# Kernel tuning notes

Hardware: AMD Instinct MI355X
Metric: run time of the kernel (lower is better)

Reference implementation:

```python
import jax, jax.numpy as jnp
import numpy as np
import math

N_QUBITS = 10
N_LAYERS = 2
HIDDEN = 768
VOCAB = 30522
DIM = 2 ** N_QUBITS


def _cnot_perm(c, t, n):
    # PennyLane convention: wire 0 is the most significant bit of the basis index.
    idx = np.arange(2 ** n)
    ctrl_bit = (idx >> (n - 1 - c)) & 1
    return jnp.asarray(idx ^ (ctrl_bit << (n - 1 - t)))

# BasicEntanglerLayers uses a CNOT ring: (0,1),(1,2),...,(n-1,0)
CNOT_PERMS = [_cnot_perm(q, (q + 1) % N_QUBITS, N_QUBITS) for q in range(N_QUBITS)]


def _apply_rx(state, theta, q):
    # state: (N, 2^n) complex, theta: (N,) per-sample RX angle on wire q.
    c = jnp.cos(theta * 0.5)[:, None, None]
    s = jnp.sin(theta * 0.5)[:, None, None]
    st = state.reshape(-1, 2 ** q, 2, DIM // (2 ** (q + 1)))
    a0, a1 = st[:, :, 0, :], st[:, :, 1, :]
    b0 = c * a0 - 1j * s * a1
    b1 = c * a1 - 1j * s * a0
    return jnp.stack([b0, b1], axis=2).reshape(state.shape)


def _quantum_probs(angles):
    # angles: (N, L, n). BasicEntanglerLayers = per-layer RX rotations + CNOT ring,
    # followed by qml.probs over all wires -> (N, 2^n).
    N = angles.shape[0]
    state = jnp.zeros((N, DIM), jnp.complex64).at[:, 0].set(1.0)
    for l in range(N_LAYERS):
        for q in range(N_QUBITS):
            state = _apply_rx(state, angles[:, l, q], q)
        for q in range(N_QUBITS):
            state = state[:, CNOT_PERMS[q]]
    return state.real ** 2 + state.imag ** 2


def _gelu(x):
    return x * 0.5 * (1.0 + jax.scipy.special.erf(x / math.sqrt(2.0)))


def setup_inputs() -> dict:
    key = jax.random.key(0)
    ks = jax.random.split(key, 4)
    B, S = 8, 512
    return {
        "hidden_states": jax.random.normal(ks[0], (B, S, HIDDEN), jnp.float32),
        "dense_w": jax.random.normal(ks[1], (HIDDEN, HIDDEN), jnp.float32) * 0.02,
        "dense_b": jnp.zeros((HIDDEN,), jnp.float32),
        "ln_w": jnp.ones((HIDDEN,), jnp.float32),
        "ln_b": jnp.zeros((HIDDEN,), jnp.float32),
        "ent_w": jax.random.normal(ks[2], (HIDDEN, N_LAYERS * N_QUBITS), jnp.float32) * 0.02,
        "ent_b": jnp.zeros((N_LAYERS * N_QUBITS,), jnp.float32),
        "proj_w": jax.random.normal(ks[3], (DIM, VOCAB), jnp.float32) * 0.02,
        "proj_b": jnp.zeros((VOCAB,), jnp.float32),
    }


def reference(hidden_states, dense_w, dense_b, ln_w, ln_b, ent_w, ent_b, proj_w, proj_b):
    # BertPredictionHeadTransform: dense -> gelu -> LayerNorm (eps inside sqrt)
    h = _gelu(hidden_states @ dense_w + dense_b)
    u = h.mean(-1, keepdims=True)
    v = ((h - u) ** 2).mean(-1, keepdims=True)
    h = ln_w * ((h - u) / jnp.sqrt(v + 1e-12)) + ln_b
    # entangle params -> sigmoid * 2pi, flatten batch to (N, L, n)
    ang = jax.nn.sigmoid(h @ ent_w + ent_b).reshape(-1, N_LAYERS, N_QUBITS) * (2.0 * math.pi)
    probs = _quantum_probs(ang)  # (B*S, 2^n)
    return probs @ proj_w + proj_b  # (B*S, vocab)
```

## Files before the change

### kernel.cpp

```cpp
#include <hip/hip_runtime.h>
#include <hip/hip_bf16.h>
#include <math.h>

#define HIDDEN 768
#define NROWS 4096
#define QDIM 1024
#define VOCAB 30522
#define NPAD 30592
#define NBX 239
#define NBY 32
#define NWG (NBX * NBY)
#define NT (QDIM / 64)

typedef _Float16 half8 __attribute__((ext_vector_type(8)));
typedef float floatx4 __attribute__((ext_vector_type(4)));
typedef float floatx2 __attribute__((ext_vector_type(2)));

__device__ __forceinline__ void gload16(const _Float16* g, _Float16* l) {
  __builtin_amdgcn_global_load_lds(
      (const __attribute__((address_space(1))) void*)g,
      (__attribute__((address_space(3))) void*)l, 16, 0, 0);
}

__global__ __launch_bounds__(1024) void convert_transpose(
    const float* __restrict__ B, _Float16* __restrict__ BT) {
  __shared__ _Float16 tile[32][33];
  int n0 = blockIdx.x * 32;
  int k0 = blockIdx.y * 32;
  int tx = threadIdx.x, ty = threadIdx.y;
  int n = n0 + tx, k = k0 + ty;
  float v = (n < VOCAB) ? B[k * VOCAB + n] : 0.0f;
  tile[ty][tx] = (_Float16)v;
  __syncthreads();
  BT[(n0 + ty) * QDIM + (k0 + tx)] = tile[tx][ty];
}

__global__ __launch_bounds__(256) void gemm1_gelu(
    const float* __restrict__ A, const float* __restrict__ W,
    const float* __restrict__ bias, float* __restrict__ H) {
  __shared__ float As[64][17];
  __shared__ float Bs[16][68];
  int t = threadIdx.x;
  int bm = blockIdx.y * 64, bn = blockIdx.x * 64;
  int tx = t & 15, ty = t >> 4;
  float acc[4][4] = {};
  for (int k0 = 0; k0 < HIDDEN; k0 += 16) {
    {
      int r = t >> 2, c = (t & 3) * 4;
      float4 v = *(const float4*)&A[(bm + r) * HIDDEN + k0 + c];
      As[r][c] = v.x; As[r][c + 1] = v.y; As[r][c + 2] = v.z; As[r][c + 3] = v.w;
    }
    {
      int kr = t >> 4, c = (t & 15) * 4;
      float4 v = *(const float4*)&W[(k0 + kr) * HIDDEN + bn + c];
      Bs[kr][c] = v.x; Bs[kr][c + 1] = v.y; Bs[kr][c + 2] = v.z; Bs[kr][c + 3] = v.w;
    }
    __syncthreads();
#pragma unroll
    for (int k = 0; k < 16; k++) {
      float a[4], b[4];
#pragma unroll
      for (int i = 0; i < 4; i++) a[i] = As[ty * 4 + i][k];
#pragma unroll
      for (int j = 0; j < 4; j++) b[j] = Bs[k][tx * 4 + j];
#pragma unroll
      for (int i = 0; i < 4; i++)
#pragma unroll
        for (int j = 0; j < 4; j++) acc[i][j] += a[i] * b[j];
    }
    __syncthreads();
  }
#pragma unroll
  for (int i = 0; i < 4; i++) {
    int m = bm + ty * 4 + i;
#pragma unroll
    for (int j = 0; j < 4; j++) {
      int n = bn + tx * 4 + j;
      float x = acc[i][j] + bias[n];
      float g = x * 0.5f * (1.0f + erff(x * 0.70710678118654752f));
      H[m * HIDDEN + n] = g;
    }
  }
}

__device__ inline float block_sum256(float v, float* red) {
  int t = threadIdx.x;
#pragma unroll
  for (int o = 32; o > 0; o >>= 1) v += __shfl_down(v, o);
  __syncthreads();
  if ((t & 63) == 0) red[t >> 6] = v;
  __syncthreads();
  return red[0] + red[1] + red[2] + red[3];
}

__global__ __launch_bounds__(256) void row_quantum(
    const float* __restrict__ H, const float* __restrict__ ln_w,
    const float* __restrict__ ln_b, const float* __restrict__ ent_w,
    const float* __restrict__ ent_b, _Float16* __restrict__ probsA) {
  __shared__ float hn[HIDDEN];
  __shared__ float red[4];
  __shared__ float sr[QDIM];
  __shared__ float si[QDIM];
  __shared__ float ang[20];
  int t = threadIdx.x;
  int row = blockIdx.x;
  const float* hr = H + row * HIDDEN;

  float sum = 0.f;
  for (int i = t; i < HIDDEN; i += 256) {
    float v = hr[i];
    hn[i] = v;
    sum += v;
  }
  float u = block_sum256(sum, red) * (1.0f / HIDDEN);
  float vs = 0.f;
  for (int i = t; i < HIDDEN; i += 256) {
    float d = hn[i] - u;
    vs += d * d;
  }
  float var = block_sum256(vs, red) * (1.0f / HIDDEN);
  float inv = rsqrtf(var + 1e-12f);
  for (int i = t; i < HIDDEN; i += 256)
    hn[i] = ln_w[i] * ((hn[i] - u) * inv) + ln_b[i];
  __syncthreads();

  {
    int w = t >> 6, lane = t & 63;
#pragma unroll
    for (int kk = 0; kk < 5; kk++) {
      int o = w * 5 + kk;
      float p = 0.f;
#pragma unroll
      for (int i = 0; i < HIDDEN / 64; i++)
        p += hn[lane + i * 64] * ent_w[(lane + i * 64) * 20 + o];
#pragma unroll
      for (int off = 32; off > 0; off >>= 1) p += __shfl_down(p, off);
      if (lane == 0) {
        float acc = p + ent_b[o];
        float s = 1.0f / (1.0f + expf(-acc));
        ang[o] = 6.283185307179586f * s;
      }
    }
  }
  __syncthreads();

  for (int i = t; i < QDIM; i += 256) {
    sr[i] = (i == 0) ? 1.0f : 0.0f;
    si[i] = 0.0f;
  }
  __syncthreads();

  for (int l = 0; l < 2; l++) {
    for (int q = 0; q < 10; q++) {
      float th = ang[l * 10 + q] * 0.5f;
      float c = cosf(th), s = sinf(th);
      int bp = 9 - q;
      int mask = 1 << bp;
#pragma unroll
      for (int p = 0; p < 2; p++) {
        int pi = t + p * 256;
        int i0 = ((pi >> bp) << (bp + 1)) | (pi & (mask - 1));
        int i1 = i0 | mask;
        float a0r = sr[i0], a0i = si[i0], a1r = sr[i1], a1i = si[i1];
        sr[i0] = c * a0r + s * a1i;
        si[i0] = c * a0i - s * a1r;
        sr[i1] = c * a1r + s * a0i;
        si[i1] = c * a1i - s * a0r;
      }
      __syncthreads();
    }
    float tr[4], ti[4];
#pragma unroll
    for (int p = 0; p < 4; p++) {
      int i = t + p * 256;
      int j = i;
#pragma unroll
      for (int q = 9; q >= 0; q--) {
        int cb = 9 - q;
        int tb = 9 - ((q + 1) % 10);
        j ^= ((j >> cb) & 1) << tb;
      }
      tr[p] = sr[j];
      ti[p] = si[j];
    }
    __syncthreads();
#pragma unroll
    for (int p = 0; p < 4; p++) {
      int i = t + p * 256;
      sr[i] = tr[p];
      si[i] = ti[p];
    }
    __syncthreads();
  }

  for (int i = t; i < QDIM; i += 256) {
    float pv = sr[i] * sr[i] + si[i] * si[i];
    probsA[row * QDIM + i] = (_Float16)pv;
  }
}

__global__ __launch_bounds__(256) void gemm2_mfma(
    const _Float16* __restrict__ A,
    const _Float16* __restrict__ BT,
    const float* __restrict__ bias,
    float* __restrict__ C) {
  __shared__ __align__(16) char smem_raw[65536];
  auto As = (_Float16 (*)[128][64])(smem_raw);
  auto Bs = (_Float16 (*)[128][64])(smem_raw + 32768);

  int t = threadIdx.x;
  int lane = t & 63, wave = t >> 6;
  int quad = lane >> 4, ln = lane & 15;
  int wm = (wave >> 1) * 64, wn = (wave & 1) * 64;

  int wg = blockIdx.x;
  int swz = (wg & 7) * (NWG / 8) + (wg >> 3);
  int bn = (swz >> 5) * 128;
  int bm = (swz & 31) * 128;

  int srow = t >> 3;
  int ps = t & 7;
  int lslot = ps ^ (srow & 7);
  const _Float16* gA = A  + (size_t)(bm + srow) * QDIM + lslot * 8;
  const _Float16* gB = BT + (size_t)(bn + srow) * QDIM + lslot * 8;

  int r7 = ln & 7;
  int off0 = ((0 * 4 + quad) ^ r7) * 8;
  int off1 = ((1 * 4 + quad) ^ r7) * 8;

  floatx4 acc[4][4];
#pragma unroll
  for (int i = 0; i < 4; i++)
#pragma unroll
    for (int j = 0; j < 4; j++) acc[i][j] = (floatx4){0.f, 0.f, 0.f, 0.f};

  auto STAGE = [&](int kt, int b) {
#pragma unroll
    for (int i = 0; i < 4; i++) {
      gload16(gA + (size_t)i * 32 * QDIM + kt * 64, &As[b][srow + i * 32][ps * 8]);
      gload16(gB + (size_t)i * 32 * QDIM + kt * 64, &Bs[b][srow + i * 32][ps * 8]);
    }
  };

  auto COMPUTE = [&](int b) {
    __builtin_amdgcn_s_setprio(1);
#pragma unroll
    for (int s = 0; s < 2; s++) {
      int off = s ? off1 : off0;
      half8 a[4], bb[4];
#pragma unroll
      for (int i = 0; i < 4; i++) a[i] = *(const half8*)&As[b][wm + i * 16 + ln][off];
#pragma unroll
      for (int j = 0; j < 4; j++) bb[j] = *(const half8*)&Bs[b][wn + j * 16 + ln][off];
#pragma unroll
      for (int i = 0; i < 4; i++)
#pragma unroll
        for (int j = 0; j < 4; j++)
          acc[i][j] = __builtin_amdgcn_mfma_f32_16x16x32_f16(a[i], bb[j], acc[i][j], 0, 0, 0);
    }
    __builtin_amdgcn_s_setprio(0);
  };

  STAGE(0, 0);
  int cur = 0;
  for (int kt = 0; kt < NT - 1; ++kt) {
    STAGE(kt + 1, cur ^ 1);
    asm volatile("s_waitcnt vmcnt(8)" ::: "memory");
    __builtin_amdgcn_s_barrier();
    COMPUTE(cur);
    __builtin_amdgcn_s_barrier();
    cur ^= 1;
  }
  asm volatile("s_waitcnt vmcnt(0)" ::: "memory");
  __builtin_amdgcn_s_barrier();
  COMPUTE(cur);

  __syncthreads();
  float* ctile = (float*)smem_raw;
#pragma unroll
  for (int j = 0; j < 4; j++)
#pragma unroll
    for (int i = 0; i < 4; i++)
#pragma unroll
      for (int r = 0; r < 4; r++)
        ctile[(wm + i * 16 + quad * 4 + r) * 128 + wn + j * 16 + ln] = acc[i][j][r];
  __syncthreads();

  if (bn + 128 <= VOCAB) {
#pragma unroll 4
    for (int idx = t; idx < 8192; idx += 256) {
      int row = idx >> 6;
      int c2 = (idx & 63) * 2;
      floatx2 v = *(const floatx2*)&ctile[row * 128 + c2];
      floatx2 bv = *(const floatx2*)&bias[bn + c2];
      v[0] += bv[0]; v[1] += bv[1];
      __builtin_nontemporal_store(
          v, (floatx2*)&C[(size_t)(bm + row) * VOCAB + bn + c2]);
    }
  } else {
    for (int idx = t; idx < 8192; idx += 256) {
      int row = idx >> 6;
      int c2 = (idx & 63) * 2;
#pragma unroll
      for (int e = 0; e < 2; e++) {
        int n = bn + c2 + e;
        if (n < VOCAB)
          C[(size_t)(bm + row) * VOCAB + n] = ctile[row * 128 + c2 + e] + bias[n];
      }
    }
  }
}

extern "C" void kernel_launch(void* const* d_in, const int* in_sizes, int n_in,
                              void* d_out, int out_size, void* d_ws, size_t ws_size,
                              hipStream_t stream) {
  const float* hs      = (const float*)d_in[0];
  const float* dense_w = (const float*)d_in[1];
  const float* dense_b = (const float*)d_in[2];
  const float* ln_w    = (const float*)d_in[3];
  const float* ln_b    = (const float*)d_in[4];
  const float* ent_w   = (const float*)d_in[5];
  const float* ent_b   = (const float*)d_in[6];
  const float* proj_w  = (const float*)d_in[7];
  const float* proj_b  = (const float*)d_in[8];
  float* out = (float*)d_out;

  char* ws = (char*)d_ws;
  float*     h      = (float*)ws;
  _Float16*  probsA = (_Float16*)(ws + 12582912);
  _Float16*  BT     = (_Float16*)(ws + 20971520);

  hipLaunchKernelGGL(convert_transpose, dim3(NPAD / 32, QDIM / 32), dim3(32, 32), 0, stream,
                     proj_w, BT);
  hipLaunchKernelGGL(gemm1_gelu, dim3(HIDDEN / 64, NROWS / 64), dim3(256), 0, stream,
                     hs, dense_w, dense_b, h);
  hipLaunchKernelGGL(row_quantum, dim3(NROWS), dim3(256), 0, stream,
                     h, ln_w, ln_b, ent_w, ent_b, probsA);
  hipLaunchKernelGGL(gemm2_mfma, dim3(NWG), dim3(256), 0, stream,
                     probsA, BT, proj_b, out);
}
```

Before: 1.143 ms.

## Use split-fp16 MFMA for the dense GEMM and swizzle the gemm2 epilogue tile

Replaces the scalar fp32 dense GEMM with an MFMA kernel. Inputs and weights are split into fp16 hi/lo parts, and three MFMAs per tile pair (hi*hi, hi*lo, lo*hi) keep near-fp32 accuracy. Two new preprocessing kernels do the split, with a transpose for the weight, and the workspace is reordered so the scratch buffers reuse BT's region before convert_transpose runs. The gemm2 epilogue now XOR-swizzles the LDS C tile columns to cut bank conflicts. The cost is extra passes that convert and write the activations, and fp16 range or precision limits on the split representation.

```diff
diff --git a/kernel.cpp b/kernel.cpp
--- a/kernel.cpp
+++ b/kernel.cpp
@@ -13,10 +13,11 @@
 #define NT (QDIM / 64)
 
 typedef _Float16 half8 __attribute__((ext_vector_type(8)));
+typedef _Float16 half4 __attribute__((ext_vector_type(4)));
 typedef float floatx4 __attribute__((ext_vector_type(4)));
 typedef float floatx2 __attribute__((ext_vector_type(2)));
 
-__device__ __forceinline__ void gload16(const _Float16* g, _Float16* l) {
+__device__ __forceinline__ void gload16(const void* g, void* l) {
   __builtin_amdgcn_global_load_lds(
       (const __attribute__((address_space(1))) void*)g,
       (__attribute__((address_space(3))) void*)l, 16, 0, 0);
@@ -35,51 +36,113 @@
   BT[(n0 + ty) * QDIM + (k0 + tx)] = tile[tx][ty];
 }
 
-__global__ __launch_bounds__(256) void gemm1_gelu(
-    const float* __restrict__ A, const float* __restrict__ W,
+__global__ __launch_bounds__(256) void split_hs(
+    const float* __restrict__ X, _Float16* __restrict__ Hi, _Float16* __restrict__ Lo) {
+  int idx4 = blockIdx.x * 256 + threadIdx.x;
+  float4 v = *(const float4*)&X[idx4 * 4];
+  half4 h, l;
+  float x;
+  x = v.x; h[0] = (_Float16)x; l[0] = (_Float16)(x - (float)h[0]);
+  x = v.y; h[1] = (_Float16)x; l[1] = (_Float16)(x - (float)h[1]);
+  x = v.z; h[2] = (_Float16)x; l[2] = (_Float16)(x - (float)h[2]);
+  x = v.w; h[3] = (_Float16)x; l[3] = (_Float16)(x - (float)h[3]);
+  *(half4*)&Hi[idx4 * 4] = h;
+  *(half4*)&Lo[idx4 * 4] = l;
+}
+
+__global__ __launch_bounds__(1024) void split_wT(
+    const float* __restrict__ W, _Float16* __restrict__ Hi, _Float16* __restrict__ Lo) {
+  __shared__ float tile[32][33];
+  int n0 = blockIdx.x * 32;
+  int k0 = blockIdx.y * 32;
+  int tx = threadIdx.x, ty = threadIdx.y;
+  tile[ty][tx] = W[(k0 + ty) * HIDDEN + n0 + tx];
+  __syncthreads();
+  float x = tile[tx][ty];
+  _Float16 h = (_Float16)x;
+  _Float16 l = (_Float16)(x - (float)h);
+  Hi[(n0 + ty) * HIDDEN + k0 + tx] = h;
+  Lo[(n0 + ty) * HIDDEN + k0 + tx] = l;
+}
+
+__global__ __launch_bounds__(256) void gemm1_mfma(
+    const _Float16* __restrict__ Ah, const _Float16* __restrict__ Al,
+    const _Float16* __restrict__ Bh, const _Float16* __restrict__ Bl,
     const float* __restrict__ bias, float* __restrict__ H) {
-  __shared__ float As[64][17];
-  __shared__ float Bs[16][68];
+  __shared__ _Float16 sAh[64][64], sAl[64][64], sBh[64][64], sBl[64][64];
   int t = threadIdx.x;
+  int lane = t & 63, wave = t >> 6;
+  int quad = lane >> 4, ln = lane & 15;
+  int wm = (wave >> 1) * 32, wn = (wave & 1) * 32;
   int bm = blockIdx.y * 64, bn = blockIdx.x * 64;
-  int tx = t & 15, ty = t >> 4;
-  float acc[4][4] = {};
-  for (int k0 = 0; k0 < HIDDEN; k0 += 16) {
-    {
-      int r = t >> 2, c = (t & 3) * 4;
-      float4 v = *(const float4*)&A[(bm + r) * HIDDEN + k0 + c];
-      As[r][c] = v.x; As[r][c + 1] = v.y; As[r][c + 2] = v.z; As[r][c + 3] = v.w;
-    }
-    {
-      int kr = t >> 4, c = (t & 15) * 4;
-      float4 v = *(const float4*)&W[(k0 + kr) * HIDDEN + bn + c];
-      Bs[kr][c] = v.x; Bs[kr][c + 1] = v.y; Bs[kr][c + 2] = v.z; Bs[kr][c + 3] = v.w;
+
+  int srow = t >> 3;
+  int ps = t & 7;
+  int lslot = ps ^ (srow & 7);
+  const _Float16* gAh = Ah + (size_t)(bm + srow) * HIDDEN + lslot * 8;
+  const _Float16* gAl = Al + (size_t)(bm + srow) * HIDDEN + lslot * 8;
+  const _Float16* gBh = Bh + (size_t)(bn + srow) * HIDDEN + lslot * 8;
+  const _Float16* gBl = Bl + (size_t)(bn + srow) * HIDDEN + lslot * 8;
+
+  int r7 = ln & 7;
+  int off0 = ((0 * 4 + quad) ^ r7) * 8;
+  int off1 = ((1 * 4 + quad) ^ r7) * 8;
+
+  floatx4 acc[2][2];
+#pragma unroll
+  for (int i = 0; i < 2; i++)
+#pragma unroll
+    for (int j = 0; j < 2; j++) acc[i][j] = (floatx4){0.f, 0.f, 0.f, 0.f};
+
+  for (int k0 = 0; k0 < HIDDEN; k0 += 64) {
+    if (k0) __syncthreads();
+#pragma unroll
+    for (int i = 0; i < 2; i++) {
+      int ro = i * 32;
+      gload16(gAh + (size_t)ro * HIDDEN + k0, &sAh[srow + ro][ps * 8]);
+      gload16(gAl + (size_t)ro * HIDDEN + k0, &sAl[srow + ro][ps * 8]);
+      gload16(gBh + (size_t)ro * HIDDEN + k0, &sBh[srow + ro][ps * 8]);
+      gload16(gBl + (size_t)ro * HIDDEN + k0, &sBl[srow + ro][ps * 8]);
     }
     __syncthreads();
 #pragma unroll
-    for (int k = 0; k < 16; k++) {
-      float a[4], b[4];
-#pragma unroll
-      for (int i = 0; i < 4; i++) a[i] = As[ty * 4 + i][k];
-#pragma unroll
-      for (int j = 0; j < 4; j++) b[j] = Bs[k][tx * 4 + j];
-#pragma unroll
-      for (int i = 0; i < 4; i++)
-#pragma unroll
-        for (int j = 0; j < 4; j++) acc[i][j] += a[i] * b[j];
-    }
-    __syncthreads();
-  }
-#pragma unroll
-  for (int i = 0; i < 4; i++) {
-    int m = bm + ty * 4 + i;
-#pragma unroll
-    for (int j = 0; j < 4; j++) {
-      int n = bn + tx * 4 + j;
-      float x = acc[i][j] + bias[n];
-      float g = x * 0.5f * (1.0f + erff(x * 0.70710678118654752f));
-      H[m * HIDDEN + n] = g;
-    }
+    for (int s = 0; s < 2; s++) {
+      int off = s ? off1 : off0;
+      half8 ah[2], al[2], bh[2], bl[2];
+#pragma unroll
+      for (int i = 0; i < 2; i++) {
+        ah[i] = *(const half8*)&sAh[wm + i * 16 + ln][off];
+        al[i] = *(const half8*)&sAl[wm + i * 16 + ln][off];
+      }
+#pragma unroll
+      for (int j = 0; j < 2; j++) {
+        bh[j] = *(const half8*)&sBh[wn + j * 16 + ln][off];
+        bl[j] = *(const half8*)&sBl[wn + j * 16 + ln][off];
+      }
+#pragma unroll
+      for (int i = 0; i < 2; i++)
+#pragma unroll
+        for (int j = 0; j < 2; j++) {
+          acc[i][j] = __builtin_amdgcn_mfma_f32_16x16x32_f16(ah[i], bh[j], acc[i][j], 0, 0, 0);
+          acc[i][j] = __builtin_amdgcn_mfma_f32_16x16x32_f16(ah[i], bl[j], acc[i][j], 0, 0, 0);
+          acc[i][j] = __builtin_amdgcn_mfma_f32_16x16x32_f16(al[i], bh[j], acc[i][j], 0, 0, 0);
+        }
+    }
+  }
+
+#pragma unroll
+  for (int j = 0; j < 2; j++) {
+    int n = bn + wn + j * 16 + ln;
+    float bv = bias[n];
+#pragma unroll
+    for (int i = 0; i < 2; i++)
+#pragma unroll
+      for (int r = 0; r < 4; r++) {
+        int m = bm + wm + i * 16 + quad * 4 + r;
+        float x = acc[i][j][r] + bv;
+        float g = x * 0.5f * (1.0f + erff(x * 0.70710678118654752f));
+        H[(size_t)m * HIDDEN + n] = g;
+      }
   }
 }
 
@@ -282,8 +345,11 @@
 #pragma unroll
     for (int i = 0; i < 4; i++)
 #pragma unroll
-      for (int r = 0; r < 4; r++)
-        ctile[(wm + i * 16 + quad * 4 + r) * 128 + wn + j * 16 + ln] = acc[i][j][r];
+      for (int r = 0; r < 4; r++) {
+        int row = wm + i * 16 + quad * 4 + r;
+        int col = (wn + j * 16 + ln) ^ (((row >> 2) & 3) << 4);
+        ctile[row * 128 + col] = acc[i][j][r];
+      }
   __syncthreads();
 
   if (bn + 128 <= VOCAB) {
@@ -291,7 +357,8 @@
     for (int idx = t; idx < 8192; idx += 256) {
       int row = idx >> 6;
       int c2 = (idx & 63) * 2;
-      floatx2 v = *(const floatx2*)&ctile[row * 128 + c2];
+      int pc = c2 ^ (((row >> 2) & 3) << 4);
+      floatx2 v = *(const floatx2*)&ctile[row * 128 + pc];
       floatx2 bv = *(const floatx2*)&bias[bn + c2];
       v[0] += bv[0]; v[1] += bv[1];
       __builtin_nontemporal_store(
@@ -301,11 +368,12 @@
     for (int idx = t; idx < 8192; idx += 256) {
       int row = idx >> 6;
       int c2 = (idx & 63) * 2;
+      int pc = c2 ^ (((row >> 2) & 3) << 4);
 #pragma unroll
       for (int e = 0; e < 2; e++) {
         int n = bn + c2 + e;
         if (n < VOCAB)
-          C[(size_t)(bm + row) * VOCAB + n] = ctile[row * 128 + c2 + e] + bias[n];
+          C[(size_t)(bm + row) * VOCAB + n] = ctile[row * 128 + pc + e] + bias[n];
       }
     }
   }
@@ -329,13 +397,21 @@
   float*     h      = (float*)ws;
   _Float16*  probsA = (_Float16*)(ws + 12582912);
   _Float16*  BT     = (_Float16*)(ws + 20971520);
-
+  _Float16*  Ahi = (_Float16*)(ws + 20971520);
+  _Float16*  Alo = (_Float16*)(ws + 27262976);
+  _Float16*  WThi = (_Float16*)(ws + 33554432);
+  _Float16*  WTlo = (_Float16*)(ws + 34734080);
+
+  hipLaunchKernelGGL(split_hs, dim3(NROWS * HIDDEN / 1024), dim3(256), 0, stream,
+                     hs, Ahi, Alo);
+  hipLaunchKernelGGL(split_wT, dim3(HIDDEN / 32, HIDDEN / 32), dim3(32, 32), 0, stream,
+                     dense_w, WThi, WTlo);
+  hipLaunchKernelGGL(gemm1_mfma, dim3(HIDDEN / 64, NROWS / 64), dim3(256), 0, stream,
+                     Ahi, Alo, WThi, WTlo, dense_b, h);
+  hipLaunchKernelGGL(row_quantum, dim3(NROWS), dim3(256), 0, stream,
+                     h, ln_w, ln_b, ent_w, ent_b, probsA);
   hipLaunchKernelGGL(convert_transpose, dim3(NPAD / 32, QDIM / 32), dim3(32, 32), 0, stream,
                      proj_w, BT);
-  hipLaunchKernelGGL(gemm1_gelu, dim3(HIDDEN / 64, NROWS / 64), dim3(256), 0, stream,
-                     hs, dense_w, dense_b, h);
-  hipLaunchKernelGGL(row_quantum, dim3(NROWS), dim3(256), 0, stream,
-                     h, ln_w, ln_b, ent_w, ent_b, probsA);
   hipLaunchKernelGGL(gemm2_mfma, dim3(NWG), dim3(256), 0, stream,
                      probsA, BT, proj_b, out);
 }
```

Result: faster. 1.089 ms (-4.8%).
